# Kernel optimization log

Hardware: AMD Instinct MI355X
Metric: run time of the kernel (lower is better)

## Reference

```python
import jax, jax.numpy as jnp
import numpy as np

B, N, C, H = 8, 4096, 768, 8
EPS = 1e-12  # F.normalize eps


def setup_inputs() -> dict:
    key = jax.random.key(0)
    ks = jax.random.split(key, 4)
    x = jax.random.normal(ks[0], (B, N, C), dtype=jnp.float32)
    w_qkv = jax.random.normal(ks[1], (3 * C, C), dtype=jnp.float32) * 0.02
    temperature = jnp.ones((H, 1, 1), dtype=jnp.float32)
    w_proj = jax.random.normal(ks[2], (C, C), dtype=jnp.float32) * 0.02
    b_proj = jnp.zeros((C,), dtype=jnp.float32)
    return {"x": x, "w_qkv": w_qkv, "temperature": temperature,
            "w_proj": w_proj, "b_proj": b_proj}


def _l2norm(t):
    # F.normalize(t, dim=-1): t / max(||t||_2, eps)
    n = jnp.sqrt(jnp.sum(t * t, axis=-1, keepdims=True))
    return t / jnp.maximum(n, EPS)


def reference(x, w_qkv, temperature, w_proj, b_proj):
    b, n, c = x.shape
    h = H
    hd = c // h
    # qkv projection: (B,N,3C) -> (3,B,H,hd,N)
    qkv = (x @ w_qkv.T).reshape(b, n, 3, h, hd)
    qkv = jnp.transpose(qkv, (2, 0, 3, 4, 1))
    q, k, v = qkv[0], qkv[1], qkv[2]          # each (B,H,hd,N)
    qn = _l2norm(q)                            # normalize over N (token) dim
    kn = _l2norm(k)
    # small per-head covariance attention: (B,H,hd,hd)
    attn = jnp.einsum('bhdn,bhen->bhde', qn, kn) * temperature
    attn = jax.nn.softmax(attn, axis=-1)
    out = jnp.einsum('bhde,bhen->bhdn', attn, v)  # (B,H,hd,N)
    out = jnp.transpose(out, (0, 3, 1, 2)).reshape(b, n, c)
    return out @ w_proj.T + b_proj
```

## Files before the change

### kernel.cpp

```cpp
#include <hip/hip_runtime.h>
#include <cstdint>
#include <cstddef>

#define B_ 8
#define N_ 4096
#define C_ 768
#define H_ 8
#define HD_ 96
#define EPSN 1e-12f
#define NS_ 4

typedef short s16x8 __attribute__((ext_vector_type(8)));
typedef short s16x4 __attribute__((ext_vector_type(4)));
typedef float f32x4 __attribute__((ext_vector_type(4)));

static __device__ __forceinline__ short f2bf(float f) {
  unsigned u = __float_as_uint(f);
  unsigned r = (u + 0x7fff + ((u >> 16) & 1)) >> 16;
  return (short)r;
}
static __device__ __forceinline__ float bf2f(unsigned short s) {
  return __uint_as_float(((unsigned)s) << 16);
}
static __device__ __forceinline__ s16x8 pack8(const float4 a, const float4 b) {
  s16x8 r;
  r[0] = f2bf(a.x); r[1] = f2bf(a.y); r[2] = f2bf(a.z); r[3] = f2bf(a.w);
  r[4] = f2bf(b.x); r[5] = f2bf(b.y); r[6] = f2bf(b.z); r[7] = f2bf(b.w);
  return r;
}

#define TSW(ch, t) ((t) ^ ((((ch) >> 2) & 7) << 3))

__global__ __launch_bounds__(256)
void gram_p(const float* __restrict__ x, float* __restrict__ Gp) {
  const int f = blockIdx.x;
  const int xcd = f & 7;
  const int t = f >> 3;
  const int pair = t % 21;
  const int cdiv = t / 21;
  const int c = xcd + 8 * cdiv;
  const int split = c & 3;
  const int b = c >> 2;

  int rem = pair, ti = 0;
#pragma unroll
  for (int it = 0; it < 5; ++it)
    if (rem >= 6 - ti) { rem -= 6 - ti; ++ti; }
  const int tj = ti + rem;
  const int i0 = ti * 128, j0 = tj * 128;
  const bool diag = (ti == tj);

  const int tid = threadIdx.x;
  const int lane = tid & 63, wave = tid >> 6;
  const int l15 = lane & 15, quad = lane >> 4;
  const int wm = wave & 1, wn = wave >> 1;

  __shared__ __align__(16) short smem[2 * 128 * 72];
  short* At = smem;
  short* Bt = smem + 128 * 72;

  const int tg = tid >> 4;
  const int cg = tid & 15;
  const int t0 = tg * 4;
  const int c0 = cg * 4;
  const float* xb = x + (size_t)b * N_ * C_;

  f32x4 acc[4][4] = {};

  const int nbeg = split * (N_ / NS_);
  const int nend = nbeg + (N_ / NS_);
  for (int n0 = nbeg; n0 < nend; n0 += 64) {
    float4 la[2][4], lb[2][4];
#pragma unroll
    for (int q = 0; q < 2; ++q)
#pragma unroll
      for (int r = 0; r < 4; ++r)
        la[q][r] = *(const float4*)(xb + (size_t)(n0 + t0 + r) * C_ + i0 + c0 + q * 64);
    if (!diag) {
#pragma unroll
      for (int q = 0; q < 2; ++q)
#pragma unroll
        for (int r = 0; r < 4; ++r)
          lb[q][r] = *(const float4*)(xb + (size_t)(n0 + t0 + r) * C_ + j0 + c0 + q * 64);
    }
    __syncthreads();
#pragma unroll
    for (int q = 0; q < 2; ++q)
#pragma unroll
      for (int cc = 0; cc < 4; ++cc) {
        const int ch = c0 + q * 64 + cc;
        s16x4 v;
        v[0] = f2bf(((const float*)&la[q][0])[cc]);
        v[1] = f2bf(((const float*)&la[q][1])[cc]);
        v[2] = f2bf(((const float*)&la[q][2])[cc]);
        v[3] = f2bf(((const float*)&la[q][3])[cc]);
        *(s16x4*)&At[ch * 72 + TSW(ch, t0)] = v;
      }
    if (!diag) {
#pragma unroll
      for (int q = 0; q < 2; ++q)
#pragma unroll
        for (int cc = 0; cc < 4; ++cc) {
          const int ch = c0 + q * 64 + cc;
          s16x4 v;
          v[0] = f2bf(((const float*)&lb[q][0])[cc]);
          v[1] = f2bf(((const float*)&lb[q][1])[cc]);
          v[2] = f2bf(((const float*)&lb[q][2])[cc]);
          v[3] = f2bf(((const float*)&lb[q][3])[cc]);
          *(s16x4*)&Bt[ch * 72 + TSW(ch, t0)] = v;
        }
    }
    __syncthreads();
    const short* Bre = diag ? At : Bt;
#pragma unroll
    for (int ks = 0; ks < 64; ks += 32) {
      s16x8 af[4], bfr[4];
#pragma unroll
      for (int mi = 0; mi < 4; ++mi) {
        const int ch = wm * 64 + mi * 16 + l15;
        af[mi] = *(const s16x8*)&At[ch * 72 + TSW(ch, ks + quad * 8)];
      }
#pragma unroll
      for (int ni = 0; ni < 4; ++ni) {
        const int ch = wn * 64 + ni * 16 + l15;
        bfr[ni] = *(const s16x8*)&Bre[ch * 72 + TSW(ch, ks + quad * 8)];
      }
#pragma unroll
      for (int ni = 0; ni < 4; ++ni)
#pragma unroll
        for (int mi = 0; mi < 4; ++mi)
          acc[mi][ni] = __builtin_amdgcn_mfma_f32_16x16x32_bf16(af[mi], bfr[ni], acc[mi][ni], 0, 0, 0);
    }
  }

  float* Gpb = Gp + (((size_t)b * 21 + pair) * NS_ + split) * (128 * 128);
#pragma unroll
  for (int mi = 0; mi < 4; ++mi)
#pragma unroll
    for (int ni = 0; ni < 4; ++ni) {
      const int ii = wm * 64 + mi * 16 + quad * 4;
      const int jj = wn * 64 + ni * 16 + l15;
#pragma unroll
      for (int r = 0; r < 4; ++r)
        Gpb[(ii + r) * 128 + jj] = acc[mi][ni][r];
    }
}

__global__ __launch_bounds__(256)
void gram_red(const float* __restrict__ Gp, short* __restrict__ G) {
  const int pair = blockIdx.x;
  int rem = pair, ti = 0;
#pragma unroll
  for (int it = 0; it < 5; ++it)
    if (rem >= 6 - ti) { rem -= 6 - ti; ++ti; }
  const int tj = ti + rem;
  const int b = blockIdx.y;
  const int i0 = ti * 128, j0 = tj * 128;
  const bool diag = (ti == tj);
  const int tid = threadIdx.x;

  __shared__ short Ts[128 * 137];

  const float4* P = (const float4*)(Gp + (((size_t)b * 21 + pair) * NS_) * (128 * 128));
  short* Gb = G + (size_t)b * C_ * C_;

#pragma unroll
  for (int it = 0; it < 16; ++it) {
    const int q = tid + it * 256;
    const int row = q >> 5;
    const int c4 = q & 31;
    float4 v = P[q];
    const float4 v1 = P[q + 4096];
    const float4 v2 = P[q + 8192];
    const float4 v3 = P[q + 12288];
    v.x += v1.x + v2.x + v3.x;
    v.y += v1.y + v2.y + v3.y;
    v.z += v1.z + v2.z + v3.z;
    v.w += v1.w + v2.w + v3.w;
    s16x4 sv;
    sv[0] = f2bf(v.x); sv[1] = f2bf(v.y); sv[2] = f2bf(v.z); sv[3] = f2bf(v.w);
    *(s16x4*)&Gb[(size_t)(i0 + row) * C_ + j0 + c4 * 4] = sv;
    if (!diag) {
#pragma unroll
      for (int c = 0; c < 4; ++c)
        Ts[(c4 * 4 + c) * 137 + row] = sv[c];
    }
  }
  if (!diag) {
    __syncthreads();
#pragma unroll
    for (int p = 0; p < 8; ++p) {
      const int id = tid + p * 256;
      const int j = id >> 4, cs = (id & 15) * 8;
      *(s16x8*)&Gb[(size_t)(j0 + j) * C_ + i0 + cs] = *(const s16x8*)&Ts[j * 137 + cs];
    }
  }
}

__global__ __launch_bounds__(256)
void gemm_fb(const float* __restrict__ A, const short* __restrict__ Bb,
             short* __restrict__ Out, size_t sB, size_t sO) {
  const int z = blockIdx.z;
  const int n0 = blockIdx.x * 128;
  const int m0 = blockIdx.y * 128;
  const int tid = threadIdx.x;
  const int lane = tid & 63, wave = tid >> 6;
  const int l15 = lane & 15, quad = lane >> 4;
  const int wm = wave & 1, wn = wave >> 1;

  __shared__ __align__(16) short As[128 * 40];
  __shared__ __align__(16) short Bs[128 * 40];

  const int ar = tid >> 1;
  const int ak = (tid & 1) * 16;
  const float* ap = A + (size_t)(m0 + ar) * C_ + ak;
  const short* bp = Bb + (size_t)z * sB + (size_t)(n0 + ar) * C_ + ak;

  f32x4 acc[4][4] = {};

  for (int k0 = 0; k0 < C_; k0 += 32) {
    const float4 a0 = *(const float4*)(ap + k0 + 0);
    const float4 a1 = *(const float4*)(ap + k0 + 4);
    const float4 a2 = *(const float4*)(ap + k0 + 8);
    const float4 a3 = *(const float4*)(ap + k0 + 12);
    const s16x8 b0 = *(const s16x8*)(bp + k0 + 0);
    const s16x8 b1 = *(const s16x8*)(bp + k0 + 8);
    __syncthreads();
    *(s16x8*)&As[ar * 40 + ak]     = pack8(a0, a1);
    *(s16x8*)&As[ar * 40 + ak + 8] = pack8(a2, a3);
    *(s16x8*)&Bs[ar * 40 + ak]     = b0;
    *(s16x8*)&Bs[ar * 40 + ak + 8] = b1;
    __syncthreads();
    s16x8 af[4];
#pragma unroll
    for (int mi = 0; mi < 4; ++mi)
      af[mi] = *(const s16x8*)&As[(wm * 64 + mi * 16 + l15) * 40 + quad * 8];
#pragma unroll
    for (int ni = 0; ni < 4; ++ni) {
      const s16x8 bf = *(const s16x8*)&Bs[(wn * 64 + ni * 16 + l15) * 40 + quad * 8];
#pragma unroll
      for (int mi = 0; mi < 4; ++mi)
        acc[mi][ni] = __builtin_amdgcn_mfma_f32_16x16x32_bf16(af[mi], bf, acc[mi][ni], 0, 0, 0);
    }
  }

  short* ob = Out + (size_t)z * sO;
#pragma unroll
  for (int mi = 0; mi < 4; ++mi) {
    const int m = m0 + wm * 64 + mi * 16 + quad * 4;
#pragma unroll
    for (int ni = 0; ni < 4; ++ni) {
      const int n = n0 + wn * 64 + ni * 16 + l15;
#pragma unroll
      for (int r = 0; r < 4; ++r)
        ob[(size_t)(m + r) * C_ + n] = f2bf(acc[mi][ni][r]);
    }
  }
}

__global__ __launch_bounds__(256)
void row_norms(const short* __restrict__ Y, const float* __restrict__ w_qkv,
               float* __restrict__ norms) {
  const int b = blockIdx.y;
  const int m = blockIdx.x * 4 + (threadIdx.x >> 6);
  const int lane = threadIdx.x & 63;
  const short* y = Y + ((size_t)b * 1536 + m) * C_;
  const float* w = w_qkv + (size_t)m * C_;
  float s = 0.f;
#pragma unroll
  for (int j = 0; j < 3; ++j) {
    const int o = j * 256 + lane * 4;
    const s16x4 yv = *(const s16x4*)(y + o);
    const float4 wv = *(const float4*)(w + o);
    s += bf2f((unsigned short)yv[0]) * wv.x + bf2f((unsigned short)yv[1]) * wv.y +
         bf2f((unsigned short)yv[2]) * wv.z + bf2f((unsigned short)yv[3]) * wv.w;
  }
#pragma unroll
  for (int o = 32; o > 0; o >>= 1) s += __shfl_xor(s, o);
  if (lane == 0) {
    int idx;
    if (m < 768) idx = (b * 8 + m / 96) * 96 + (m % 96);
    else { const int mm = m - 768; idx = B_ * H_ * 96 + (b * 8 + mm / 96) * 96 + (mm % 96); }
    norms[idx] = s;
  }
}

__global__ __launch_bounds__(256)
void s_attn(const short* __restrict__ Y, const float* __restrict__ w_qkv,
            const float* __restrict__ norms, const float* __restrict__ temp,
            float* __restrict__ S) {
  const int bh = blockIdx.x;
  const int b = bh >> 3, h = bh & 7;
  const int tid = threadIdx.x;
  const int lane = tid & 63, wave = tid >> 6;
  const int l15 = lane & 15, quad = lane >> 4;

  __shared__ __align__(16) float Sf[96 * 97];
  __shared__ float qsc[96], ksc[96];
  short* Ys = (short*)Sf;
  short* Ks = (short*)Sf + 96 * 72;

  if (tid < 96)
    qsc[tid] = temp[h] / fmaxf(sqrtf(norms[bh * 96 + tid]), EPSN);
  else if (tid < 192)
    ksc[tid - 96] = 1.0f / fmaxf(sqrtf(norms[B_ * H_ * 96 + bh * 96 + (tid - 96)]), EPSN);

  const short* yb = Y + ((size_t)b * 1536 + h * 96) * C_;
  const float* wk = w_qkv + (size_t)(C_ + h * 96) * C_;

  f32x4 sc[9] = {};
  for (int k0 = 0; k0 < C_; k0 += 64) {
    s16x8 yv[3];
    float4 wv[3][2];
#pragma unroll
    for (int j = 0; j < 3; ++j) {
      const int id = tid + j * 256;
      const int r = id >> 3, c8 = (id & 7) * 8;
      yv[j] = *(const s16x8*)(yb + (size_t)r * C_ + k0 + c8);
      wv[j][0] = *(const float4*)(wk + (size_t)r * C_ + k0 + c8);
      wv[j][1] = *(const float4*)(wk + (size_t)r * C_ + k0 + c8 + 4);
    }
    __syncthreads();
#pragma unroll
    for (int j = 0; j < 3; ++j) {
      const int id = tid + j * 256;
      const int r = id >> 3, c8 = (id & 7) * 8;
      *(s16x8*)&Ys[r * 72 + c8] = yv[j];
      *(s16x8*)&Ks[r * 72 + c8] = pack8(wv[j][0], wv[j][1]);
    }
    __syncthreads();
#pragma unroll
    for (int j = 0; j < 9; ++j) {
      const int t = wave * 9 + j, dt = t / 6, et = t % 6;
#pragma unroll
      for (int kk = 0; kk < 64; kk += 32) {
        const s16x8 a  = *(const s16x8*)&Ys[(dt * 16 + l15) * 72 + kk + quad * 8];
        const s16x8 bb = *(const s16x8*)&Ks[(et * 16 + l15) * 72 + kk + quad * 8];
        sc[j] = __builtin_amdgcn_mfma_f32_16x16x32_bf16(a, bb, sc[j], 0, 0, 0);
      }
    }
  }
  __syncthreads();
#pragma unroll
  for (int j = 0; j < 9; ++j) {
    const int t = wave * 9 + j, dt = t / 6, et = t % 6;
    const int e = et * 16 + l15;
    const float kf = ksc[e];
#pragma unroll
    for (int r = 0; r < 4; ++r) {
      const int d = dt * 16 + quad * 4 + r;
      Sf[d * 97 + e] = sc[j][r] * qsc[d] * kf;
    }
  }
  __syncthreads();
  float* Sb = S + (size_t)bh * (HD_ * HD_);
  for (int rr = 0; rr < 24; ++rr) {
    const int d = wave * 24 + rr;
    const float v0 = Sf[d * 97 + lane];
    const float v1 = (lane < 32) ? Sf[d * 97 + 64 + lane] : -1e30f;
    float mx = fmaxf(v0, v1);
#pragma unroll
    for (int o = 32; o > 0; o >>= 1) mx = fmaxf(mx, __shfl_xor(mx, o));
    const float e0 = __expf(v0 - mx);
    const float e1 = (lane < 32) ? __expf(v1 - mx) : 0.0f;
    float sum = e0 + e1;
#pragma unroll
    for (int o = 32; o > 0; o >>= 1) sum += __shfl_xor(sum, o);
    const float inv = 1.0f / sum;
    Sb[d * 96 + lane] = e0 * inv;
    if (lane < 32) Sb[d * 96 + 64 + lane] = e1 * inv;
  }
}

__global__ __launch_bounds__(256)
void av_gemm(const float* __restrict__ S, const float* __restrict__ w_qkv,
             short* __restrict__ AVt) {
  const int bh = blockIdx.x;
  const int b = bh >> 3, h = bh & 7;
  const int ct = blockIdx.y * 64;
  const int tid = threadIdx.x;
  __shared__ float at[96 * 97];
  __shared__ float wv[96 * 64];
  const float* Sb = S + (size_t)bh * (HD_ * HD_);
  for (int i = tid; i < 96 * 96; i += 256)
    at[(i / 96) * 97 + (i % 96)] = Sb[i];
  for (int i = tid; i < 96 * 64; i += 256) {
    const int e = i >> 6, c = i & 63;
    wv[e * 64 + c] = w_qkv[(size_t)(2 * C_ + h * 96 + e) * C_ + ct + c];
  }
  __syncthreads();
  const int d0 = (tid >> 4) * 6;
  const int c0 = (tid & 15) * 4;
  float acc[6][4] = {};
  for (int e = 0; e < 96; ++e) {
    const float4 bv = *(const float4*)&wv[e * 64 + c0];
    float aa[6];
#pragma unroll
    for (int i = 0; i < 6; ++i) aa[i] = at[(d0 + i) * 97 + e];
#pragma unroll
    for (int i = 0; i < 6; ++i) {
      acc[i][0] += aa[i] * bv.x; acc[i][1] += aa[i] * bv.y;
      acc[i][2] += aa[i] * bv.z; acc[i][3] += aa[i] * bv.w;
    }
  }
  short* AVb = AVt + (size_t)b * C_ * C_;
#pragma unroll
  for (int i = 0; i < 6; ++i)
#pragma unroll
    for (int j = 0; j < 4; ++j)
      AVb[(size_t)(ct + c0 + j) * C_ + h * 96 + d0 + i] = f2bf(acc[i][j]);
}

__global__ __launch_bounds__(256)
void gemm_xm(const float* __restrict__ x, const short* __restrict__ Mb,
             const float* __restrict__ bias, float* __restrict__ out) {
  const int f = blockIdx.x;
  const int xcd = f & 7;
  const int t = f >> 3;
  const int j6 = t % 6;
  const int sdiv = t / 6;
  const int s = xcd + 8 * sdiv;
  const int z = s >> 5;
  const int n0 = j6 * 128;
  const int m0 = (s & 31) * 128;
  const int tid = threadIdx.x;
  const int lane = tid & 63;
  const int wave = tid >> 6;
  const int l15 = lane & 15;
  const int quad = lane >> 4;
  const int wm = wave & 1;
  const int wn = wave >> 1;

  __shared__ __align__(16) short As[128 * 40];
  __shared__ __align__(16) short Bs[128 * 40];

  const int ar = tid >> 1;
  const int ak = (tid & 1) * 16;
  const float* xp = x + ((size_t)z * N_ + m0 + ar) * C_ + ak;
  const short* mp = Mb + (size_t)z * C_ * C_ + (size_t)(n0 + ar) * C_ + ak;

  f32x4 acc[4][4] = {};

  for (int k0 = 0; k0 < C_; k0 += 32) {
    const float4 a0 = *(const float4*)(xp + k0 + 0);
    const float4 a1 = *(const float4*)(xp + k0 + 4);
    const float4 a2 = *(const float4*)(xp + k0 + 8);
    const float4 a3 = *(const float4*)(xp + k0 + 12);
    const s16x8 b0 = *(const s16x8*)(mp + k0 + 0);
    const s16x8 b1 = *(const s16x8*)(mp + k0 + 8);
    __syncthreads();
    *(s16x8*)&As[ar * 40 + ak]     = pack8(a0, a1);
    *(s16x8*)&As[ar * 40 + ak + 8] = pack8(a2, a3);
    *(s16x8*)&Bs[ar * 40 + ak]     = b0;
    *(s16x8*)&Bs[ar * 40 + ak + 8] = b1;
    __syncthreads();
    s16x8 af[4];
#pragma unroll
    for (int mi = 0; mi < 4; ++mi)
      af[mi] = *(const s16x8*)&As[(wm * 64 + mi * 16 + l15) * 40 + quad * 8];
#pragma unroll
    for (int ni = 0; ni < 4; ++ni) {
      const s16x8 bf = *(const s16x8*)&Bs[(wn * 64 + ni * 16 + l15) * 40 + quad * 8];
#pragma unroll
      for (int mi = 0; mi < 4; ++mi)
        acc[mi][ni] = __builtin_amdgcn_mfma_f32_16x16x32_bf16(af[mi], bf, acc[mi][ni], 0, 0, 0);
    }
  }

  float bv[4];
#pragma unroll
  for (int ni = 0; ni < 4; ++ni) bv[ni] = bias[n0 + wn * 64 + ni * 16 + l15];
#pragma unroll
  for (int mi = 0; mi < 4; ++mi) {
    const int m = m0 + wm * 64 + mi * 16 + quad * 4;
#pragma unroll
    for (int ni = 0; ni < 4; ++ni) {
      const int n = n0 + wn * 64 + ni * 16 + l15;
      float* dst = out + ((size_t)z * N_ + m) * C_ + n;
#pragma unroll
      for (int r = 0; r < 4; ++r)
        dst[(size_t)r * C_] = acc[mi][ni][r] + bv[ni];
    }
  }
}

extern "C" void kernel_launch(void* const* d_in, const int* in_sizes, int n_in,
                              void* d_out, int out_size, void* d_ws, size_t ws_size,
                              hipStream_t stream) {
  const float* x      = (const float*)d_in[0];
  const float* w_qkv  = (const float*)d_in[1];
  const float* temp   = (const float*)d_in[2];
  const float* w_proj = (const float*)d_in[3];
  const float* b_proj = (const float*)d_in[4];
  float* out = (float*)d_out;

  float* ws    = (float*)d_ws;
  float* S     = ws;
  float* norms = S + (size_t)B_ * H_ * HD_ * HD_;
  short* G     = (short*)(norms + 2 * B_ * H_ * HD_);
  short* AVt   = G;
  short* Mb    = G + (size_t)B_ * C_ * C_;
  short* Y     = Mb + (size_t)B_ * C_ * C_;
  float* Gp    = (float*)Mb;

  gram_p<<<21 * NS_ * B_, 256, 0, stream>>>(x, Gp);

  gram_red<<<dim3(21, B_), 256, 0, stream>>>(Gp, G);

  gemm_fb<<<dim3(C_ / 128, 1536 / 128, B_), 256, 0, stream>>>(
      w_qkv, G, Y, (size_t)C_ * C_, (size_t)1536 * C_);

  row_norms<<<dim3(1536 / 4, B_), 256, 0, stream>>>(Y, w_qkv, norms);

  s_attn<<<B_ * H_, 256, 0, stream>>>(Y, w_qkv, norms, temp, S);

  av_gemm<<<dim3(B_ * H_, C_ / 64), 256, 0, stream>>>(S, w_qkv, AVt);

  gemm_fb<<<dim3(C_ / 128, C_ / 128, B_), 256, 0, stream>>>(
      w_proj, AVt, Mb, (size_t)C_ * C_, (size_t)C_ * C_);

  gemm_xm<<<C_ / 128 * (N_ / 128) * B_, 256, 0, stream>>>(x, Mb, b_proj, out);
}
```

Before: 430.9 us.

## Pre-convert x to bf16 once and use direct global-to-LDS loads in GEMMs

Adds a conversion kernel that writes x as bf16 into the workspace, so the Gram and final x·M GEMMs read half the bytes and skip per-tile fp32-to-bf16 packing. The final GEMM and the bf16 B-operand path of gemm_fb now use global_load_lds directly into a swizzled, unpadded LDS tile. Workspace-size tiers pick which path runs, falling back to the fp32 kernels when the workspace is too small. The extra conversion pass costs one full read of x plus a bf16 write, which must be repaid by the cheaper later reads.

```diff
diff --git a/kernel.cpp b/kernel.cpp
--- a/kernel.cpp
+++ b/kernel.cpp
@@ -31,8 +31,30 @@
 
 #define TSW(ch, t) ((t) ^ ((((ch) >> 2) & 7) << 3))
 
-__global__ __launch_bounds__(256)
-void gram_p(const float* __restrict__ x, float* __restrict__ Gp) {
+static __device__ __forceinline__ int swz(int s) {
+  return s ^ (((s >> 7) & 3) << 3);
+}
+
+static __device__ __forceinline__ void gld16(const short* g, short* l) {
+  __builtin_amdgcn_global_load_lds(
+      (const __attribute__((address_space(1))) void*)g,
+      (__attribute__((address_space(3))) void*)l, 16, 0, 0);
+}
+
+__global__ __launch_bounds__(256)
+void xcvt(const float* __restrict__ x, short* __restrict__ xb) {
+  const int n8 = (B_ * N_ * C_) / 8;
+  for (int i = blockIdx.x * 256 + threadIdx.x; i < n8; i += gridDim.x * 256) {
+    const float4 a = *(const float4*)(x + (size_t)i * 8);
+    const float4 b = *(const float4*)(x + (size_t)i * 8 + 4);
+    *(s16x8*)(xb + (size_t)i * 8) = pack8(a, b);
+  }
+}
+
+template<int BF>
+__global__ __launch_bounds__(256)
+void gram_p(const float* __restrict__ x, const short* __restrict__ xb,
+            float* __restrict__ Gp) {
   const int f = blockIdx.x;
   const int xcd = f & 7;
   const int t = f >> 3;
@@ -63,54 +85,85 @@
   const int cg = tid & 15;
   const int t0 = tg * 4;
   const int c0 = cg * 4;
-  const float* xb = x + (size_t)b * N_ * C_;
+  const float* xbF = x + (size_t)b * N_ * C_;
+  const short* xbB = xb + (size_t)b * N_ * C_;
 
   f32x4 acc[4][4] = {};
 
   const int nbeg = split * (N_ / NS_);
   const int nend = nbeg + (N_ / NS_);
   for (int n0 = nbeg; n0 < nend; n0 += 64) {
-    float4 la[2][4], lb[2][4];
-#pragma unroll
-    for (int q = 0; q < 2; ++q)
+    if (BF) {
+      s16x8 la[4], lb[4];
 #pragma unroll
       for (int r = 0; r < 4; ++r)
-        la[q][r] = *(const float4*)(xb + (size_t)(n0 + t0 + r) * C_ + i0 + c0 + q * 64);
-    if (!diag) {
+        la[r] = *(const s16x8*)(xbB + (size_t)(n0 + t0 + r) * C_ + i0 + cg * 8);
+      if (!diag) {
+#pragma unroll
+        for (int r = 0; r < 4; ++r)
+          lb[r] = *(const s16x8*)(xbB + (size_t)(n0 + t0 + r) * C_ + j0 + cg * 8);
+      }
+      __syncthreads();
+#pragma unroll
+      for (int cc = 0; cc < 8; ++cc) {
+        const int ch = cg * 8 + cc;
+        s16x4 v;
+        v[0] = la[0][cc]; v[1] = la[1][cc]; v[2] = la[2][cc]; v[3] = la[3][cc];
+        *(s16x4*)&At[ch * 72 + TSW(ch, t0)] = v;
+      }
+      if (!diag) {
+#pragma unroll
+        for (int cc = 0; cc < 8; ++cc) {
+          const int ch = cg * 8 + cc;
+          s16x4 v;
+          v[0] = lb[0][cc]; v[1] = lb[1][cc]; v[2] = lb[2][cc]; v[3] = lb[3][cc];
+          *(s16x4*)&Bt[ch * 72 + TSW(ch, t0)] = v;
+        }
+      }
+      __syncthreads();
+    } else {
+      float4 la[2][4], lb[2][4];
 #pragma unroll
       for (int q = 0; q < 2; ++q)
 #pragma unroll
         for (int r = 0; r < 4; ++r)
-          lb[q][r] = *(const float4*)(xb + (size_t)(n0 + t0 + r) * C_ + j0 + c0 + q * 64);
-    }
-    __syncthreads();
-#pragma unroll
-    for (int q = 0; q < 2; ++q)
-#pragma unroll
-      for (int cc = 0; cc < 4; ++cc) {
-        const int ch = c0 + q * 64 + cc;
-        s16x4 v;
-        v[0] = f2bf(((const float*)&la[q][0])[cc]);
-        v[1] = f2bf(((const float*)&la[q][1])[cc]);
-        v[2] = f2bf(((const float*)&la[q][2])[cc]);
-        v[3] = f2bf(((const float*)&la[q][3])[cc]);
-        *(s16x4*)&At[ch * 72 + TSW(ch, t0)] = v;
-      }
-    if (!diag) {
+          la[q][r] = *(const float4*)(xbF + (size_t)(n0 + t0 + r) * C_ + i0 + c0 + q * 64);
+      if (!diag) {
+#pragma unroll
+        for (int q = 0; q < 2; ++q)
+#pragma unroll
+          for (int r = 0; r < 4; ++r)
+            lb[q][r] = *(const float4*)(xbF + (size_t)(n0 + t0 + r) * C_ + j0 + c0 + q * 64);
+      }
+      __syncthreads();
 #pragma unroll
       for (int q = 0; q < 2; ++q)
 #pragma unroll
         for (int cc = 0; cc < 4; ++cc) {
           const int ch = c0 + q * 64 + cc;
           s16x4 v;
-          v[0] = f2bf(((const float*)&lb[q][0])[cc]);
-          v[1] = f2bf(((const float*)&lb[q][1])[cc]);
-          v[2] = f2bf(((const float*)&lb[q][2])[cc]);
-          v[3] = f2bf(((const float*)&lb[q][3])[cc]);
-          *(s16x4*)&Bt[ch * 72 + TSW(ch, t0)] = v;
+          v[0] = f2bf(((const float*)&la[q][0])[cc]);
+          v[1] = f2bf(((const float*)&la[q][1])[cc]);
+          v[2] = f2bf(((const float*)&la[q][2])[cc]);
+          v[3] = f2bf(((const float*)&la[q][3])[cc]);
+          *(s16x4*)&At[ch * 72 + TSW(ch, t0)] = v;
         }
-    }
-    __syncthreads();
+      if (!diag) {
+#pragma unroll
+        for (int q = 0; q < 2; ++q)
+#pragma unroll
+          for (int cc = 0; cc < 4; ++cc) {
+            const int ch = c0 + q * 64 + cc;
+            s16x4 v;
+            v[0] = f2bf(((const float*)&lb[q][0])[cc]);
+            v[1] = f2bf(((const float*)&lb[q][1])[cc]);
+            v[2] = f2bf(((const float*)&lb[q][2])[cc]);
+            v[3] = f2bf(((const float*)&lb[q][3])[cc]);
+            *(s16x4*)&Bt[ch * 72 + TSW(ch, t0)] = v;
+          }
+      }
+      __syncthreads();
+    }
     const short* Bre = diag ? At : Bt;
 #pragma unroll
     for (int ks = 0; ks < 64; ks += 32) {
@@ -131,6 +184,7 @@
         for (int mi = 0; mi < 4; ++mi)
           acc[mi][ni] = __builtin_amdgcn_mfma_f32_16x16x32_bf16(af[mi], bfr[ni], acc[mi][ni], 0, 0, 0);
     }
+    if (BF) __syncthreads();
   }
 
   float* Gpb = Gp + (((size_t)b * 21 + pair) * NS_ + split) * (128 * 128);
@@ -209,12 +263,21 @@
   const int wm = wave & 1, wn = wave >> 1;
 
   __shared__ __align__(16) short As[128 * 40];
-  __shared__ __align__(16) short Bs[128 * 40];
+  __shared__ __align__(16) short Bs[128 * 32];
 
   const int ar = tid >> 1;
   const int ak = (tid & 1) * 16;
   const float* ap = A + (size_t)(m0 + ar) * C_ + ak;
-  const short* bp = Bb + (size_t)z * sB + (size_t)(n0 + ar) * C_ + ak;
+
+  const short* bsrc[2];
+  short* bdst[2];
+#pragma unroll
+  for (int cc = 0; cc < 2; ++cc) {
+    const int P = wave * 1024 + cc * 512 + lane * 8;
+    const int L = swz(P);
+    bsrc[cc] = Bb + (size_t)z * sB + (size_t)(n0 + (L >> 5)) * C_ + (L & 31);
+    bdst[cc] = &Bs[wave * 1024 + cc * 512];
+  }
 
   f32x4 acc[4][4] = {};
 
@@ -223,13 +286,11 @@
     const float4 a1 = *(const float4*)(ap + k0 + 4);
     const float4 a2 = *(const float4*)(ap + k0 + 8);
     const float4 a3 = *(const float4*)(ap + k0 + 12);
-    const s16x8 b0 = *(const s16x8*)(bp + k0 + 0);
-    const s16x8 b1 = *(const s16x8*)(bp + k0 + 8);
-    __syncthreads();
+    __syncthreads();
+#pragma unroll
+    for (int cc = 0; cc < 2; ++cc) gld16(bsrc[cc] + k0, bdst[cc]);
     *(s16x8*)&As[ar * 40 + ak]     = pack8(a0, a1);
     *(s16x8*)&As[ar * 40 + ak + 8] = pack8(a2, a3);
-    *(s16x8*)&Bs[ar * 40 + ak]     = b0;
-    *(s16x8*)&Bs[ar * 40 + ak + 8] = b1;
     __syncthreads();
     s16x8 af[4];
 #pragma unroll
@@ -237,7 +298,7 @@
       af[mi] = *(const s16x8*)&As[(wm * 64 + mi * 16 + l15) * 40 + quad * 8];
 #pragma unroll
     for (int ni = 0; ni < 4; ++ni) {
-      const s16x8 bf = *(const s16x8*)&Bs[(wn * 64 + ni * 16 + l15) * 40 + quad * 8];
+      const s16x8 bf = *(const s16x8*)&Bs[swz((wn * 64 + ni * 16 + l15) * 32 + quad * 8)];
 #pragma unroll
       for (int mi = 0; mi < 4; ++mi)
         acc[mi][ni] = __builtin_amdgcn_mfma_f32_16x16x32_bf16(af[mi], bf, acc[mi][ni], 0, 0, 0);
@@ -412,8 +473,8 @@
 }
 
 __global__ __launch_bounds__(256)
-void gemm_xm(const float* __restrict__ x, const short* __restrict__ Mb,
-             const float* __restrict__ bias, float* __restrict__ out) {
+void gemm_xm_bf(const short* __restrict__ xb, const short* __restrict__ Mb,
+                const float* __restrict__ bias, float* __restrict__ out) {
   const int f = blockIdx.x;
   const int xcd = f & 7;
   const int t = f >> 3;
@@ -431,6 +492,82 @@
   const int wm = wave & 1;
   const int wn = wave >> 1;
 
+  __shared__ __align__(16) short As[128 * 32];
+  __shared__ __align__(16) short Bs[128 * 32];
+
+  const short* asrc[2]; const short* bsrc[2];
+  short* adst[2]; short* bdst[2];
+#pragma unroll
+  for (int cc = 0; cc < 2; ++cc) {
+    const int P = wave * 1024 + cc * 512 + lane * 8;
+    const int L = swz(P);
+    const int row = L >> 5, col = L & 31;
+    asrc[cc] = xb + ((size_t)z * N_ + m0 + row) * C_ + col;
+    bsrc[cc] = Mb + (size_t)z * C_ * C_ + (size_t)(n0 + row) * C_ + col;
+    adst[cc] = &As[wave * 1024 + cc * 512];
+    bdst[cc] = &Bs[wave * 1024 + cc * 512];
+  }
+
+  f32x4 acc[4][4] = {};
+
+  for (int k0 = 0; k0 < C_; k0 += 32) {
+    __syncthreads();
+#pragma unroll
+    for (int cc = 0; cc < 2; ++cc) {
+      gld16(asrc[cc] + k0, adst[cc]);
+      gld16(bsrc[cc] + k0, bdst[cc]);
+    }
+    __syncthreads();
+    s16x8 af[4];
+#pragma unroll
+    for (int mi = 0; mi < 4; ++mi)
+      af[mi] = *(const s16x8*)&As[swz((wm * 64 + mi * 16 + l15) * 32 + quad * 8)];
+#pragma unroll
+    for (int ni = 0; ni < 4; ++ni) {
+      const s16x8 bf = *(const s16x8*)&Bs[swz((wn * 64 + ni * 16 + l15) * 32 + quad * 8)];
+#pragma unroll
+      for (int mi = 0; mi < 4; ++mi)
+        acc[mi][ni] = __builtin_amdgcn_mfma_f32_16x16x32_bf16(af[mi], bf, acc[mi][ni], 0, 0, 0);
+    }
+  }
+
+  float bv[4];
+#pragma unroll
+  for (int ni = 0; ni < 4; ++ni) bv[ni] = bias[n0 + wn * 64 + ni * 16 + l15];
+#pragma unroll
+  for (int mi = 0; mi < 4; ++mi) {
+    const int m = m0 + wm * 64 + mi * 16 + quad * 4;
+#pragma unroll
+    for (int ni = 0; ni < 4; ++ni) {
+      const int n = n0 + wn * 64 + ni * 16 + l15;
+      float* dst = out + ((size_t)z * N_ + m) * C_ + n;
+#pragma unroll
+      for (int r = 0; r < 4; ++r)
+        dst[(size_t)r * C_] = acc[mi][ni][r] + bv[ni];
+    }
+  }
+}
+
+__global__ __launch_bounds__(256)
+void gemm_xm_f32(const float* __restrict__ x, const short* __restrict__ Mb,
+                 const float* __restrict__ bias, float* __restrict__ out) {
+  const int f = blockIdx.x;
+  const int xcd = f & 7;
+  const int t = f >> 3;
+  const int j6 = t % 6;
+  const int sdiv = t / 6;
+  const int s = xcd + 8 * sdiv;
+  const int z = s >> 5;
+  const int n0 = j6 * 128;
+  const int m0 = (s & 31) * 128;
+  const int tid = threadIdx.x;
+  const int lane = tid & 63;
+  const int wave = tid >> 6;
+  const int l15 = lane & 15;
+  const int quad = lane >> 4;
+  const int wm = wave & 1;
+  const int wn = wave >> 1;
+
   __shared__ __align__(16) short As[128 * 40];
   __shared__ __align__(16) short Bs[128 * 40];
 
@@ -494,18 +631,32 @@
   const float* b_proj = (const float*)d_in[4];
   float* out = (float*)d_out;
 
-  float* ws    = (float*)d_ws;
-  float* S     = ws;
-  float* norms = S + (size_t)B_ * H_ * HD_ * HD_;
-  short* G     = (short*)(norms + 2 * B_ * H_ * HD_);
+  char* base = (char*)d_ws;
+  float* S     = (float*)base;
+  float* norms = (float*)(base + 2359296);
+  short* G     = (short*)(base + 2408448);
   short* AVt   = G;
-  short* Mb    = G + (size_t)B_ * C_ * C_;
-  short* Y     = Mb + (size_t)B_ * C_ * C_;
-  float* Gp    = (float*)Mb;
-
-  gram_p<<<21 * NS_ * B_, 256, 0, stream>>>(x, Gp);
+  short* Mb    = (short*)(base + 11845632);
+  short* Y     = (short*)(base + 21282816);
+
+  const size_t need1 = 55885824 + 50331648;
+  const size_t need2 = 40157184 + 50331648;
+  const int tier = (ws_size >= need1) ? 1 : (ws_size >= need2) ? 2 : 3;
+
+  float* Gp = (tier == 2) ? (float*)(base + 40157184) : (float*)(base + 11845632);
+  short* xb = (tier == 1) ? (short*)(base + 55885824)
+            : (tier == 2) ? (short*)(base + 40157184) : nullptr;
+
+  if (tier == 1) {
+    xcvt<<<3072, 256, 0, stream>>>(x, xb);
+    gram_p<1><<<21 * NS_ * B_, 256, 0, stream>>>(x, xb, Gp);
+  } else {
+    gram_p<0><<<21 * NS_ * B_, 256, 0, stream>>>(x, xb ? xb : (const short*)G, Gp);
+  }
 
   gram_red<<<dim3(21, B_), 256, 0, stream>>>(Gp, G);
+
+  if (tier == 2) xcvt<<<3072, 256, 0, stream>>>(x, xb);
 
   gemm_fb<<<dim3(C_ / 128, 1536 / 128, B_), 256, 0, stream>>>(
       w_qkv, G, Y, (size_t)C_ * C_, (size_t)1536 * C_);
@@ -519,5 +670,8 @@
   gemm_fb<<<dim3(C_ / 128, C_ / 128, B_), 256, 0, stream>>>(
       w_proj, AVt, Mb, (size_t)C_ * C_, (size_t)C_ * C_);
 
-  gemm_xm<<<C_ / 128 * (N_ / 128) * B_, 256, 0, stream>>>(x, Mb, b_proj, out);
-}
+  if (tier == 3)
+    gemm_xm_f32<<<C_ / 128 * (N_ / 128) * B_, 256, 0, stream>>>(x, Mb, b_proj, out);
+  else
+    gemm_xm_bf<<<C_ / 128 * (N_ / 128) * B_, 256, 0, stream>>>(xb, Mb, b_proj, out);
+}
```

Result: no change. 430.6 us (-0.1%).
